# Kernel optimization log

Measured on AMD Instinct MI355X. Metric: run time of the kernel, lower is better.

## Reference

```python
import jax, jax.numpy as jnp
import numpy as np

N_VERTS = 20000
BATCH = 4
C_FEAT = 64
VOX = 64
N_FACES = 40000


def _lin(key, fan_in, fan_out):
    return jax.random.normal(key, (fan_in, fan_out), jnp.float32) / np.sqrt(fan_in)


def setup_inputs() -> dict:
    key = jax.random.key(0)
    ks = jax.random.split(key, 16)
    # faces -> unique directed edges, as in faces_to_edges (done host-side, static shape)
    rng = np.random.default_rng(0)
    faces = rng.integers(0, N_VERTS, (N_FACES, 3))
    e = np.concatenate([faces[:, :2], faces[:, 1:], faces[:, [0, 2]]], axis=0)
    e = np.unique(e, axis=0)
    edge_index = jnp.asarray(e.T, dtype=jnp.int32)  # [2, E]
    gdims = [(128, 256), (256, 512), (512, 1024), (1024, 512), (512, 256), (256, 128)]
    inp = {
        'features': jax.random.normal(ks[0], (BATCH, C_FEAT, VOX, VOX, VOX), jnp.float32),
        'vertices': jax.random.normal(ks[1], (N_VERTS, 3), jnp.float32),
        'edge_index': edge_index,
        'enc_W1': _lin(ks[2], 3 + C_FEAT, 256), 'enc_b1': jnp.zeros((256,), jnp.float32),
        'enc_W2': _lin(ks[3], 256, 128), 'enc_b2': jnp.zeros((128,), jnp.float32),
    }
    for i, (a, b) in enumerate(gdims):
        inp[f'gW{i+1}'] = _lin(ks[4 + i], a, b)
        inp[f'gb{i+1}'] = jnp.zeros((b,), jnp.float32)
    inp['hW1'] = _lin(ks[10], 128, 128); inp['hb1'] = jnp.zeros((128,), jnp.float32)
    inp['hW2'] = _lin(ks[11], 128, 64); inp['hb2'] = jnp.zeros((64,), jnp.float32)
    inp['hW3'] = _lin(ks[12], 64, 3); inp['hb3'] = jnp.zeros((3,), jnp.float32)
    return inp


def trilinear_sample(feat, grid):
    # feat [B,C,D,H,W]; grid [B,N,3] in [-1,1], channel order (x->W, y->H, z->D)
    # align_corners=True, padding_mode='border'
    _, C, D, H, W = feat.shape

    def per_sample(f, g):
        def un(c, s):
            return jnp.clip((c + 1.0) * 0.5 * (s - 1), 0.0, s - 1.0)
        x = un(g[:, 0], W); y = un(g[:, 1], H); z = un(g[:, 2], D)
        x0 = jnp.floor(x); y0 = jnp.floor(y); z0 = jnp.floor(z)
        wx = x - x0; wy = y - y0; wz = z - z0
        x0i = jnp.clip(x0.astype(jnp.int32), 0, W - 1); x1i = jnp.clip(x0i + 1, 0, W - 1)
        y0i = jnp.clip(y0.astype(jnp.int32), 0, H - 1); y1i = jnp.clip(y0i + 1, 0, H - 1)
        z0i = jnp.clip(z0.astype(jnp.int32), 0, D - 1); z1i = jnp.clip(z0i + 1, 0, D - 1)
        def g8(zi, yi, xi):
            return f[:, zi, yi, xi]  # [C,N]
        c00 = g8(z0i, y0i, x0i) * (1 - wx) + g8(z0i, y0i, x1i) * wx
        c01 = g8(z0i, y1i, x0i) * (1 - wx) + g8(z0i, y1i, x1i) * wx
        c10 = g8(z1i, y0i, x0i) * (1 - wx) + g8(z1i, y0i, x1i) * wx
        c11 = g8(z1i, y1i, x0i) * (1 - wx) + g8(z1i, y1i, x1i) * wx
        c0 = c00 * (1 - wy) + c01 * wy
        c1 = c10 * (1 - wy) + c11 * wy
        return (c0 * (1 - wz) + c1 * wz).T  # [N,C]

    return jax.vmap(per_sample)(feat, grid)


def _forward(features, vertices, edge_index,
             enc_W1, enc_b1, enc_W2, enc_b2,
             gWs, gbs, hW1, hb1, hW2, hb2, hW3, hb3):
    B = features.shape[0]
    N = vertices.shape[0]
    # sample_voxel_features: min/max over batch axis of identical copies -> constant grid
    vexp = jnp.broadcast_to(vertices[None], (B, N, 3))
    mn = vexp.min(axis=0, keepdims=True)
    mx = vexp.max(axis=0, keepdims=True)
    vn = 2.0 * (vexp - mn) / (mx - mn + 1e-6) - 1.0
    vn = vn / 1.5  # chamber == 0
    vfeat = trilinear_sample(features, vn)  # [B,N,C]
    x = jnp.concatenate([vexp, vfeat], axis=-1)
    x = jax.nn.relu(x @ enc_W1 + enc_b1)
    x = jax.nn.relu(x @ enc_W2 + enc_b2)  # [B,N,128]
    # PyG GCNConv: self-loops + symmetric normalization (bn layers unused in source forward)
    src = edge_index[0]
    dst = edge_index[1]
    deg = jnp.zeros((N,), x.dtype).at[dst].add(1.0) + 1.0  # includes self-loop
    dinv = 1.0 / jnp.sqrt(deg)
    nrm = dinv[src] * dinv[dst]  # [E]
    selfw = (dinv * dinv)[None, :, None]  # self-loop norm

    def gcn(h, W_, b_):
        h = h @ W_  # [B,N,Cout]
        agg = jnp.zeros_like(h).at[:, dst].add(h[:, src] * nrm[None, :, None])
        return jax.nn.relu(h * selfw + agg + b_)

    for W_, b_ in zip(gWs, gbs):
        x = gcn(x, W_, b_)
    d = jax.nn.relu(x @ hW1 + hb1)
    d = jax.nn.relu(d @ hW2 + hb2)
    d = jnp.tanh(d @ hW3 + hb3)
    d = jnp.nan_to_num(d, nan=0.0)
    return vertices[None] + jnp.clip(d, -2.5, 2.5)


def reference(features, vertices, edge_index,
              enc_W1, enc_b1, enc_W2, enc_b2,
              gW1, gb1, gW2, gb2, gW3, gb3, gW4, gb4, gW5, gb5, gW6, gb6,
              hW1, hb1, hW2, hb2, hW3, hb3):
    return _forward(features, vertices, edge_index,
                    enc_W1, enc_b1, enc_W2, enc_b2,
                    (gW1, gW2, gW3, gW4, gW5, gW6),
                    (gb1, gb2, gb3, gb4, gb5, gb6),
                    hW1, hb1, hW2, hb2, hW3, hb3)
```

## Files before the change

### kernel.cpp

```cpp
#include <hip/hip_runtime.h>
#include <math.h>

#define NV 20000
#define NV_PAD 20096
#define NB 4
#define M_TOTAL (NB * NV_PAD)
#define CF 64
#define VX 64

typedef short short8 __attribute__((ext_vector_type(8)));
typedef float floatx4 __attribute__((ext_vector_type(4)));

__device__ __forceinline__ float bf2f(unsigned int h) {
  return __uint_as_float(h << 16);
}
__device__ __forceinline__ unsigned short f2bf(float f) {
  unsigned int u = __float_as_uint(f);
  u += 0x7fffu + ((u >> 16) & 1u);
  return (unsigned short)(u >> 16);
}


__global__ void hist_dst_kernel(const int* __restrict__ dst, int E, int* __restrict__ cnt) {
  int i = blockIdx.x * blockDim.x + threadIdx.x;
  if (i < E) atomicAdd(&cnt[dst[i]], 1);
}

__global__ void scan_kernel(const int* __restrict__ cnt, int* __restrict__ rowp,
                            float* __restrict__ dinv, int n) {
  __shared__ int sdata[1024];
  __shared__ int run_s;
  if (threadIdx.x == 0) run_s = 0;
  __syncthreads();
  for (int base = 0; base < n; base += 1024) {
    int i = base + (int)threadIdx.x;
    int v = (i < n) ? cnt[i] : 0;
    sdata[threadIdx.x] = v;
    __syncthreads();
    int run = run_s;
    for (int ofs = 1; ofs < 1024; ofs <<= 1) {
      int t = (threadIdx.x >= (unsigned)ofs) ? sdata[threadIdx.x - ofs] : 0;
      __syncthreads();
      sdata[threadIdx.x] += t;
      __syncthreads();
    }
    if (i < n) {
      rowp[i] = run + sdata[threadIdx.x] - v;
      dinv[i] = 1.0f / sqrtf((float)(v + 1));
    }
    if (threadIdx.x == 1023) run_s = run + sdata[1023];
    __syncthreads();
  }
  if (threadIdx.x == 0) rowp[n] = run_s;
}

__global__ void fill_csr_kernel(const int* __restrict__ src, const int* __restrict__ dst, int E,
                                const int* __restrict__ rowp, int* __restrict__ cnt2,
                                const float* __restrict__ dinv,
                                int* __restrict__ esrc, float* __restrict__ dsrc) {
  int i = blockIdx.x * blockDim.x + threadIdx.x;
  if (i < E) {
    int d = dst[i];
    int s = src[i];
    int pos = rowp[d] + atomicAdd(&cnt2[d], 1);
    esrc[pos] = s;
    dsrc[pos] = dinv[s];
  }
}

__global__ void dinvrep_kernel(const float* __restrict__ dinv, float* __restrict__ drep) {
  int idx = blockIdx.x * blockDim.x + threadIdx.x;
  if (idx >= M_TOTAL) return;
  int n = idx % NV_PAD;
  drep[idx] = (n < NV) ? dinv[n] : 1.0f;
}

__global__ void vfeat_kernel(const float* __restrict__ feat, float* __restrict__ vfeat) {
  int t = blockIdx.x * blockDim.x + threadIdx.x;
  if (t >= NB * CF) return;
  float c = (2.0f * 0.0f / 1e-6f - 1.0f) / 1.5f;
  float pos = (c + 1.0f) * 0.5f * (float)(VX - 1);
  pos = fminf(fmaxf(pos, 0.0f), (float)(VX - 1));
  float f0 = floorf(pos);
  float w = pos - f0;
  int i0 = (int)f0;
  int i1 = i0 + 1; if (i1 > VX - 1) i1 = VX - 1;
  const float* base = feat + (size_t)t * VX * VX * VX;
  float wz[2] = {1.0f - w, w};
  int   iz[2] = {i0, i1};
  float acc = 0.0f;
  #pragma unroll
  for (int a = 0; a < 2; ++a)
    #pragma unroll
    for (int b = 0; b < 2; ++b)
      #pragma unroll
      for (int d = 0; d < 2; ++d)
        acc += wz[a] * wz[b] * wz[d] * base[(size_t)iz[a] * VX * VX + iz[b] * VX + iz[d]];
  vfeat[t] = acc;
}

__global__ void encconst_kernel(const float* __restrict__ vfeat, const float* __restrict__ W1,
                                const float* __restrict__ b1, float* __restrict__ encc) {
  int idx = blockIdx.x * blockDim.x + threadIdx.x;
  if (idx >= NB * 256) return;
  int b = idx >> 8, j = idx & 255;
  float acc = b1[j];
  #pragma unroll 8
  for (int c = 0; c < CF; ++c) acc += vfeat[b * CF + c] * W1[(3 + c) * 256 + j];
  encc[idx] = acc;
}

__global__ void enc1_kernel(const float* __restrict__ verts, const float* __restrict__ W1,
                            const float* __restrict__ encc, unsigned short* __restrict__ out) {
  int idx = blockIdx.x * blockDim.x + threadIdx.x;
  if (idx >= NV * 256) return;
  int n = idx >> 8, j = idx & 255;
  int b = blockIdx.y;
  float acc = encc[b * 256 + j]
            + verts[n * 3 + 0] * W1[0 * 256 + j]
            + verts[n * 3 + 1] * W1[1 * 256 + j]
            + verts[n * 3 + 2] * W1[2 * 256 + j];
  out[((size_t)(b * NV_PAD + n)) * 256 + j] = f2bf(fmaxf(acc, 0.0f));
}

struct WPrep {
  const float* src[9];
  unsigned short* dst[9];
};

__global__ void wprep_all_kernel(WPrep wp) {
  const int WKc[9] = {256, 128, 256, 512, 1024, 512, 256, 128, 128};
  const int WNc[9] = {128, 256, 512, 1024, 512, 256, 128, 128, 64};
  const int cum[10] = {0, 32768, 65536, 196608, 720896, 1245184, 1376256, 1409024, 1425408, 1433600};
  int idx = blockIdx.x * blockDim.x + threadIdx.x;
  if (idx >= 1433600) return;
  #pragma unroll
  for (int s = 0; s < 9; ++s) {
    if (idx >= cum[s] && idx < cum[s + 1]) {
      int local = idx - cum[s];
      int k = local / WNc[s];
      int n = local - k * WNc[s];
      wp.dst[s][(size_t)n * WKc[s] + k] = f2bf(wp.src[s][local]);
      return;
    }
  }
}

#define BM 128
#define BN 128
#define BK 64

__launch_bounds__(256, 4)
__global__ void gemm_bt_kernel(const unsigned short* __restrict__ A,
                               const unsigned short* __restrict__ Bt,
                               const float* __restrict__ bias,
                               const float* __restrict__ rowscale,
                               unsigned short* __restrict__ C,
                               int K, int Nreal, int flags) {
  __shared__ unsigned short As[BM * BK];
  __shared__ unsigned short Bs[BN * BK];
  int tid = threadIdx.x;
  int wave = tid >> 6, lane = tid & 63;

  unsigned int nwg = gridDim.x * gridDim.y;
  unsigned int orig = blockIdx.y * gridDim.x + blockIdx.x;
  unsigned int xcd = orig & 7u, pos = orig >> 3;
  unsigned int q = nwg >> 3, r = nwg & 7u;
  unsigned int wgid = (xcd < r ? xcd * (q + 1u) : r * (q + 1u) + (xcd - r) * q) + pos;
  unsigned int bx = wgid % gridDim.x;
  unsigned int by = wgid / gridDim.x;

  int mbase = by * BM;
  int nbase = bx * BN;
  int wm = (wave >> 1) * 64, wn = (wave & 1) * 64;

  floatx4 acc[4][4] = {};

  const int rowS = wave * 32 + (lane >> 3);
  const int kseg = (((lane & 7) ^ (lane >> 3)) << 3);
  const int fr = lane & 15, fq = lane >> 4;
  const int fr7 = fr & 7;

  for (int kb = 0; kb < K; kb += BK) {
    #pragma unroll
    for (int p = 0; p < 4; ++p) {
      const unsigned short* ga = A + (size_t)(mbase + rowS + p * 8) * K + kb + kseg;
      __builtin_amdgcn_global_load_lds(
          (const __attribute__((address_space(1))) void*)ga,
          (__attribute__((address_space(3))) void*)(As + wave * 2048 + p * 512), 16, 0, 0);
      const unsigned short* gb = Bt + (size_t)(nbase + rowS + p * 8) * K + kb + kseg;
      __builtin_amdgcn_global_load_lds(
          (const __attribute__((address_space(1))) void*)gb,
          (__attribute__((address_space(3))) void*)(Bs + wave * 2048 + p * 512), 16, 0, 0);
    }
    __syncthreads();
    #pragma unroll
    for (int kk = 0; kk < 2; ++kk) {
      const int fchunk = (((kk << 2) + fq) ^ fr7) << 3;
      short8 af[4], bf[4];
      #pragma unroll
      for (int i = 0; i < 4; ++i)
        af[i] = *(const short8*)(As + (wm + i * 16 + fr) * BK + fchunk);
      #pragma unroll
      for (int j = 0; j < 4; ++j)
        bf[j] = *(const short8*)(Bs + (wn + j * 16 + fr) * BK + fchunk);
      #pragma unroll
      for (int i = 0; i < 4; ++i)
        #pragma unroll
        for (int j = 0; j < 4; ++j)
          acc[i][j] = __builtin_amdgcn_mfma_f32_16x16x32_bf16(af[i], bf[j], acc[i][j], 0, 0, 0);
    }
    __syncthreads();
  }

  #pragma unroll
  for (int j = 0; j < 4; ++j) {
    int n = nbase + wn + j * 16 + fr;
    if (n >= Nreal) continue;
    float bv = (flags & 1) ? bias[n] : 0.0f;
    #pragma unroll
    for (int i = 0; i < 4; ++i) {
      #pragma unroll
      for (int r = 0; r < 4; ++r) {
        int m = mbase + wm + i * 16 + fq * 4 + r;
        float v = acc[i][j][r];
        if (flags & 4) v *= rowscale[m];
        v += bv;
        if (flags & 2) v = fmaxf(v, 0.0f);
        C[(size_t)m * Nreal + n] = f2bf(v);
      }
    }
  }
}

__global__ void gcn_gather_kernel(const uint4* __restrict__ hs8,
                                  const float* __restrict__ bias,
                                  const float* __restrict__ dinv,
                                  const int* __restrict__ rowp, const int* __restrict__ esrc,
                                  uint4* __restrict__ out, int lc8) {
  int idx = blockIdx.x * blockDim.x + threadIdx.x;
  int C8 = 1 << lc8;
  if (idx >= NV * C8) return;
  int n = idx >> lc8;
  int j = idx & (C8 - 1);
  size_t rowbase = (size_t)blockIdx.y * NV_PAD;
  uint4 u = hs8[((rowbase + n) << lc8) + j];
  float a0 = bf2f(u.x & 0xffff), a1 = bf2f(u.x >> 16);
  float a2 = bf2f(u.y & 0xffff), a3 = bf2f(u.y >> 16);
  float a4 = bf2f(u.z & 0xffff), a5 = bf2f(u.z >> 16);
  float a6 = bf2f(u.w & 0xffff), a7 = bf2f(u.w >> 16);
  int s = rowp[n], e = rowp[n + 1];
  int t = s;
  int src = (t < e) ? esrc[t] : 0;
  while (t < e) {
    uint4 v = hs8[((rowbase + src) << lc8) + j];
    ++t;
    int src_n = (t < e) ? esrc[t] : 0;
    a0 += bf2f(v.x & 0xffff); a1 += bf2f(v.x >> 16);
    a2 += bf2f(v.y & 0xffff); a3 += bf2f(v.y >> 16);
    a4 += bf2f(v.z & 0xffff); a5 += bf2f(v.z >> 16);
    a6 += bf2f(v.w & 0xffff); a7 += bf2f(v.w >> 16);
    src = src_n;
  }
  float dn = dinv[n];
  int j8 = j << 3;
  a0 = fmaxf(a0 * dn + bias[j8 + 0], 0.0f);
  a1 = fmaxf(a1 * dn + bias[j8 + 1], 0.0f);
  a2 = fmaxf(a2 * dn + bias[j8 + 2], 0.0f);
  a3 = fmaxf(a3 * dn + bias[j8 + 3], 0.0f);
  a4 = fmaxf(a4 * dn + bias[j8 + 4], 0.0f);
  a5 = fmaxf(a5 * dn + bias[j8 + 5], 0.0f);
  a6 = fmaxf(a6 * dn + bias[j8 + 6], 0.0f);
  a7 = fmaxf(a7 * dn + bias[j8 + 7], 0.0f);
  uint4 o;
  o.x = (unsigned int)f2bf(a0) | ((unsigned int)f2bf(a1) << 16);
  o.y = (unsigned int)f2bf(a2) | ((unsigned int)f2bf(a3) << 16);
  o.z = (unsigned int)f2bf(a4) | ((unsigned int)f2bf(a5) << 16);
  o.w = (unsigned int)f2bf(a6) | ((unsigned int)f2bf(a7) << 16);
  out[((rowbase + n) << lc8) + j] = o;
}

__global__ void gcn_pre_gather_kernel(const uint4* __restrict__ x8,
                                      const float* __restrict__ dinv,
                                      const int* __restrict__ rowp, const int* __restrict__ esrc,
                                      const float* __restrict__ dsrc,
                                      uint4* __restrict__ out, int lc8) {
  int idx = blockIdx.x * blockDim.x + threadIdx.x;
  int C8 = 1 << lc8;
  if (idx >= NV * C8) return;
  int n = idx >> lc8;
  int j = idx & (C8 - 1);
  size_t rowbase = (size_t)blockIdx.y * NV_PAD;
  float dn = dinv[n];
  uint4 u = x8[((rowbase + n) << lc8) + j];
  float a0 = dn * bf2f(u.x & 0xffff), a1 = dn * bf2f(u.x >> 16);
  float a2 = dn * bf2f(u.y & 0xffff), a3 = dn * bf2f(u.y >> 16);
  float a4 = dn * bf2f(u.z & 0xffff), a5 = dn * bf2f(u.z >> 16);
  float a6 = dn * bf2f(u.w & 0xffff), a7 = dn * bf2f(u.w >> 16);
  int s = rowp[n], e = rowp[n + 1];
  int t = s;
  int src = (t < e) ? esrc[t] : 0;
  float w = (t < e) ? dsrc[t] : 0.0f;
  while (t < e) {
    uint4 v = x8[((rowbase + src) << lc8) + j];
    float wv = w;
    ++t;
    src = (t < e) ? esrc[t] : 0;
    w = (t < e) ? dsrc[t] : 0.0f;
    a0 += wv * bf2f(v.x & 0xffff); a1 += wv * bf2f(v.x >> 16);
    a2 += wv * bf2f(v.y & 0xffff); a3 += wv * bf2f(v.y >> 16);
    a4 += wv * bf2f(v.z & 0xffff); a5 += wv * bf2f(v.z >> 16);
    a6 += wv * bf2f(v.w & 0xffff); a7 += wv * bf2f(v.w >> 16);
  }
  a0 *= dn; a1 *= dn; a2 *= dn; a3 *= dn;
  a4 *= dn; a5 *= dn; a6 *= dn; a7 *= dn;
  uint4 o;
  o.x = (unsigned int)f2bf(a0) | ((unsigned int)f2bf(a1) << 16);
  o.y = (unsigned int)f2bf(a2) | ((unsigned int)f2bf(a3) << 16);
  o.z = (unsigned int)f2bf(a4) | ((unsigned int)f2bf(a5) << 16);
  o.w = (unsigned int)f2bf(a6) | ((unsigned int)f2bf(a7) << 16);
  out[((rowbase + n) << lc8) + j] = o;
}

__global__ void head3_kernel(const unsigned short* __restrict__ d, const float* __restrict__ hW3,
                             const float* __restrict__ hb3, const float* __restrict__ verts,
                             float* __restrict__ out) {
  int idx = blockIdx.x * blockDim.x + threadIdx.x;
  if (idx >= NV * 3) return;
  int n = idx / 3;
  int k = idx - n * 3;
  int b = blockIdx.y;
  const unsigned short* drow = d + ((size_t)(b * NV_PAD + n)) * 64;
  float acc = hb3[k];
  #pragma unroll 8
  for (int c = 0; c < 64; ++c) acc += bf2f(drow[c]) * hW3[c * 3 + k];
  float t = tanhf(acc);
  t = fminf(fmaxf(t, -2.5f), 2.5f);
  out[(size_t)b * NV * 3 + idx] = verts[idx] + t;
}


static inline void launch_gemm(const unsigned short* A, const unsigned short* Bt,
                               const float* bias, const float* rowscale, unsigned short* C,
                               int N, int K, int flags, hipStream_t stream) {
  int Npad = (N + BN - 1) / BN * BN;
  dim3 grid(Npad / BN, M_TOTAL / BM);
  gemm_bt_kernel<<<grid, 256, 0, stream>>>(A, Bt, bias, rowscale, C, K, N, flags);
}

extern "C" void kernel_launch(void* const* d_in, const int* in_sizes, int n_in,
                              void* d_out, int out_size, void* d_ws, size_t ws_size,
                              hipStream_t stream) {
  const float* features = (const float*)d_in[0];
  const float* vertices = (const float*)d_in[1];
  const int* edge_index = (const int*)d_in[2];
  const int E = in_sizes[2] / 2;
  const int* esrc_in = edge_index;
  const int* edst_in = edge_index + E;
  const float* enc_W1 = (const float*)d_in[3];
  const float* enc_b1 = (const float*)d_in[4];
  const float* enc_W2 = (const float*)d_in[5];
  const float* enc_b2 = (const float*)d_in[6];
  const float* gW[6]; const float* gb[6];
  for (int i = 0; i < 6; ++i) { gW[i] = (const float*)d_in[7 + 2 * i]; gb[i] = (const float*)d_in[8 + 2 * i]; }
  const float* hW1 = (const float*)d_in[19]; const float* hb1 = (const float*)d_in[20];
  const float* hW2 = (const float*)d_in[21]; const float* hb2 = (const float*)d_in[22];
  const float* hW3 = (const float*)d_in[23]; const float* hb3 = (const float*)d_in[24];

  char* ws = (char*)d_ws;
  size_t off = 0;
  auto alloc = [&](size_t bytes) -> void* {
    void* p = (void*)(ws + off);
    off += (bytes + 255) & ~(size_t)255;
    return p;
  };
  unsigned short* bufA = (unsigned short*)alloc((size_t)M_TOTAL * 1024 * 2);
  unsigned short* bufB = (unsigned short*)alloc((size_t)M_TOTAL * 1024 * 2);
  float* dinv  = (float*)alloc(NV * sizeof(float));
  float* drep  = (float*)alloc(M_TOTAL * sizeof(float));
  float* vfeat = (float*)alloc(NB * CF * sizeof(float));
  float* encc  = (float*)alloc(NB * 256 * sizeof(float));
  int* cnt  = (int*)alloc(NV * sizeof(int));
  int* rowp = (int*)alloc((NV + 1) * sizeof(int));
  int* cnt2 = (int*)alloc(NV * sizeof(int));
  int* esrc = (int*)alloc((size_t)E * sizeof(int));
  float* dsrc = (float*)alloc((size_t)E * sizeof(float));
  const size_t wtsz[9] = {128 * 256, 256 * 128, 512 * 256, 1024 * 512, 512 * 1024,
                          256 * 512, 128 * 256, 128 * 128, 128 * 128};
  unsigned short* wt[9];
  {
    size_t tot = 0;
    for (int i = 0; i < 9; ++i) tot += wtsz[i];
    unsigned short* base = (unsigned short*)alloc(tot * 2);
    size_t o = 0;
    for (int i = 0; i < 9; ++i) { wt[i] = base + o; o += wtsz[i]; }
  }

  hipMemsetAsync(cnt,  0, NV * sizeof(int), stream);
  hipMemsetAsync(cnt2, 0, NV * sizeof(int), stream);
  hist_dst_kernel<<<(E + 255) / 256, 256, 0, stream>>>(edst_in, E, cnt);
  scan_kernel<<<1, 1024, 0, stream>>>(cnt, rowp, dinv, NV);
  fill_csr_kernel<<<(E + 255) / 256, 256, 0, stream>>>(esrc_in, edst_in, E, rowp, cnt2,
                                                       dinv, esrc, dsrc);
  dinvrep_kernel<<<(M_TOTAL + 255) / 256, 256, 0, stream>>>(dinv, drep);
  vfeat_kernel<<<1, 256, 0, stream>>>(features, vfeat);
  encconst_kernel<<<NB, 256, 0, stream>>>(vfeat, enc_W1, enc_b1, encc);

  WPrep wp;
  const float* wsrc[9] = {enc_W2, gW[0], gW[1], gW[2], gW[3], gW[4], gW[5], hW1, hW2};
  for (int i = 0; i < 9; ++i) { wp.src[i] = wsrc[i]; wp.dst[i] = wt[i]; }
  wprep_all_kernel<<<(1433600 + 255) / 256, 256, 0, stream>>>(wp);

  const int gout[6] = {256, 512, 1024, 512, 256, 128};
  const int gin[6]  = {128, 256, 512, 1024, 512, 256};
  const int inlc8[6] = {4, 5, 6, 7, 6, 5};
  const int outlc8[6] = {5, 6, 7, 6, 5, 4};
  const int inside[6] = {1, 1, 1, 0, 0, 0};

  dim3 e1grid((NV * 256 + 255) / 256, NB);
  enc1_kernel<<<e1grid, 256, 0, stream>>>(vertices, enc_W1, encc, bufA);
  launch_gemm(bufA, wt[0], enc_b2, nullptr, bufB, 128, 256, 1 | 2, stream);

  unsigned short* x = bufB;
  unsigned short* h = bufA;
  for (int i = 0; i < 6; ++i) {
    if (inside[i]) {
      int total8 = NV * (gin[i] / 8);
      dim3 pgrid((total8 + 255) / 256, NB);
      gcn_pre_gather_kernel<<<pgrid, 256, 0, stream>>>(
          (const uint4*)x, dinv, rowp, esrc, dsrc, (uint4*)h, inlc8[i]);
      launch_gemm(h, wt[1 + i], gb[i], nullptr, x, gout[i], gin[i], 1 | 2, stream);
    } else {
      launch_gemm(x, wt[1 + i], nullptr, drep, h, gout[i], gin[i], 4, stream);
      int total8 = NV * (gout[i] / 8);
      dim3 ggrid((total8 + 255) / 256, NB);
      gcn_gather_kernel<<<ggrid, 256, 0, stream>>>(
          (const uint4*)h, gb[i], dinv, rowp, esrc, (uint4*)x, outlc8[i]);
    }
  }
  launch_gemm(x, wt[7], hb1, nullptr, h, 128, 128, 1 | 2, stream);
  launch_gemm(h, wt[8], hb2, nullptr, x, 64, 128, 1 | 2, stream);
  dim3 hgrid((NV * 3 + 255) / 256, NB);
  head3_kernel<<<hgrid, 256, 0, stream>>>(x, hW3, hb3, vertices, (float*)d_out);
}
```

Before: 1.144 ms.

## Raise GEMM occupancy bound and vectorize head3 to one thread per vertex

Raises the GEMM kernel's launch_bounds minimum occupancy from 4 to 5 blocks per CU, pushing the compiler to cap register use so more waves fit. Separately, head3 now gives each thread one vertex and computes all three outputs from 16-byte vector loads, instead of three threads each reading the row with scalar bf16 loads. The register cap risks spills in the GEMM. The head change is small relative to total time.

Result: slower. 1.709 ms (+49.4%).

```diff
diff --git a/kernel.cpp b/kernel.cpp
--- a/kernel.cpp
+++ b/kernel.cpp
@@ -150,7 +150,7 @@
 #define BN 128
 #define BK 64
 
-__launch_bounds__(256, 4)
+__launch_bounds__(256, 5)
 __global__ void gemm_bt_kernel(const unsigned short* __restrict__ A,
                                const unsigned short* __restrict__ Bt,
                                const float* __restrict__ bias,
@@ -325,18 +325,33 @@
 __global__ void head3_kernel(const unsigned short* __restrict__ d, const float* __restrict__ hW3,
                              const float* __restrict__ hb3, const float* __restrict__ verts,
                              float* __restrict__ out) {
-  int idx = blockIdx.x * blockDim.x + threadIdx.x;
-  if (idx >= NV * 3) return;
-  int n = idx / 3;
-  int k = idx - n * 3;
+  int n = blockIdx.x * blockDim.x + threadIdx.x;
+  if (n >= NV) return;
   int b = blockIdx.y;
-  const unsigned short* drow = d + ((size_t)(b * NV_PAD + n)) * 64;
-  float acc = hb3[k];
-  #pragma unroll 8
-  for (int c = 0; c < 64; ++c) acc += bf2f(drow[c]) * hW3[c * 3 + k];
-  float t = tanhf(acc);
-  t = fminf(fmaxf(t, -2.5f), 2.5f);
-  out[(size_t)b * NV * 3 + idx] = verts[idx] + t;
+  const uint4* drow = (const uint4*)(d + ((size_t)(b * NV_PAD + n)) * 64);
+  float a0 = hb3[0], a1 = hb3[1], a2 = hb3[2];
+  #pragma unroll
+  for (int qv = 0; qv < 8; ++qv) {
+    uint4 v = drow[qv];
+    float f0 = bf2f(v.x & 0xffff), f1 = bf2f(v.x >> 16);
+    float f2 = bf2f(v.y & 0xffff), f3 = bf2f(v.y >> 16);
+    float f4 = bf2f(v.z & 0xffff), f5 = bf2f(v.z >> 16);
+    float f6 = bf2f(v.w & 0xffff), f7 = bf2f(v.w >> 16);
+    const float* w = hW3 + qv * 24;
+    a0 += f0 * w[0]  + f1 * w[3]  + f2 * w[6]  + f3 * w[9]
+        + f4 * w[12] + f5 * w[15] + f6 * w[18] + f7 * w[21];
+    a1 += f0 * w[1]  + f1 * w[4]  + f2 * w[7]  + f3 * w[10]
+        + f4 * w[13] + f5 * w[16] + f6 * w[19] + f7 * w[22];
+    a2 += f0 * w[2]  + f1 * w[5]  + f2 * w[8]  + f3 * w[11]
+        + f4 * w[14] + f5 * w[17] + f6 * w[20] + f7 * w[23];
+  }
+  float t0 = fminf(fmaxf(tanhf(a0), -2.5f), 2.5f);
+  float t1 = fminf(fmaxf(tanhf(a1), -2.5f), 2.5f);
+  float t2 = fminf(fmaxf(tanhf(a2), -2.5f), 2.5f);
+  size_t ob = (size_t)b * NV * 3 + (size_t)n * 3;
+  out[ob + 0] = verts[n * 3 + 0] + t0;
+  out[ob + 1] = verts[n * 3 + 1] + t1;
+  out[ob + 2] = verts[n * 3 + 2] + t2;
 }
 
 
@@ -440,6 +455,6 @@
   }
   launch_gemm(x, wt[7], hb1, nullptr, h, 128, 128, 1 | 2, stream);
   launch_gemm(h, wt[8], hb2, nullptr, x, 64, 128, 1 | 2, stream);
-  dim3 hgrid((NV * 3 + 255) / 256, NB);
+  dim3 hgrid((NV + 255) / 256, NB);
   head3_kernel<<<hgrid, 256, 0, stream>>>(x, hW3, hb3, vertices, (float*)d_out);
 }
```
